# Kernel optimization log

Hardware: AMD Instinct MI355X
Metric: run time of the kernel (lower is better)

The kernel has to match this reference:

```python
import jax, jax.numpy as jnp
import numpy as np

N = 500000   # occupied voxels
C = 128      # channels
K = 27       # 3x3x3 kernel offsets


def setup_inputs() -> dict:
    key = jax.random.key(0)
    ks = jax.random.split(key, 16)
    x = jax.random.normal(ks[0], (N, C), jnp.float32)
    nbr = jax.random.randint(ks[1], (N, K), 0, N, jnp.int32)   # neighbor map (hash-table lookups)
    mask = jax.random.randint(ks[2], (N, K), 0, 2) > 0          # neighbor exists
    s = lambda fan: np.float32(1.0 / np.sqrt(fan))
    C4, C2 = C // 4, C // 2
    W00 = jax.random.normal(ks[3], (C, C4), jnp.float32) * s(C)
    b00 = jax.random.normal(ks[4], (C4,), jnp.float32) * 0.01
    W01 = jax.random.normal(ks[5], (K, C4, C4), jnp.float32) * s(K * C4)
    b01 = jax.random.normal(ks[6], (C4,), jnp.float32) * 0.01
    W02 = jax.random.normal(ks[7], (C4, C2), jnp.float32) * s(C4)
    b02 = jax.random.normal(ks[8], (C2,), jnp.float32) * 0.01
    W10 = jax.random.normal(ks[9], (K, C, C4), jnp.float32) * s(K * C)
    b10 = jax.random.normal(ks[10], (C4,), jnp.float32) * 0.01
    W11 = jax.random.normal(ks[11], (K, C4, C2), jnp.float32) * s(K * C4)
    b11 = jax.random.normal(ks[12], (C2,), jnp.float32) * 0.01
    return {"x": x, "nbr": nbr, "mask": mask,
            "W00": W00, "b00": b00, "W01": W01, "b01": b01, "W02": W02, "b02": b02,
            "W10": W10, "b10": b10, "W11": W11, "b11": b11}


def _conv1(f, W, b):
    # kernel_size=1 sparse conv == per-point matmul
    return f @ W + b


def _conv3(f, nbr, mask, W, b):
    # kernel_size=3 sparse conv: gather-weight-scatter over 27 kernel maps
    acc0 = jnp.zeros((f.shape[0], W.shape[-1]), f.dtype)
    def step(acc, inp):
        idx, m, Wk = inp  # [N], [N], [Cin,Cout]
        g = jnp.where(m[:, None], f[idx], jnp.zeros((), f.dtype))
        return acc + g @ Wk, None
    out, _ = jax.lax.scan(step, acc0, (nbr.T, mask.T, W))
    return out + b


def reference(x, nbr, mask, W00, b00, W01, b01, W02, b02, W10, b10, W11, b11):
    relu = jax.nn.relu
    # branch 0: 1x1 -> relu -> 3x3 -> relu -> 1x1
    h0 = relu(_conv1(x, W00, b00))
    h0 = relu(_conv3(h0, nbr, mask, W01, b01))
    out0 = _conv1(h0, W02, b02)
    # branch 1: 3x3 -> relu -> 3x3
    h1 = relu(_conv3(x, nbr, mask, W10, b10))
    out1 = _conv3(h1, nbr, mask, W11, b11)
    # cat along channels, residual add
    return jnp.concatenate([out0, out1], axis=-1) + x
```

## Files before the change

### kernel.cpp

```cpp
#include <hip/hip_runtime.h>
#include <stdint.h>
#include <stddef.h>


typedef __attribute__((ext_vector_type(8))) short bf16x8;
typedef __attribute__((ext_vector_type(4))) float f32x4;

__device__ __forceinline__ float bf2f(uint16_t u) {
  union { uint32_t i; float f; } v; v.i = ((uint32_t)u) << 16; return v.f;
}
__device__ __forceinline__ uint16_t f2bf(float f) {
  union { float f; uint32_t i; } v; v.f = f;
  return (uint16_t)((v.i + 0x7fffu + ((v.i >> 16) & 1u)) >> 16);
}
__device__ __forceinline__ bf16x8 zero8() {
  bf16x8 z = {0, 0, 0, 0, 0, 0, 0, 0};
  return z;
}
__device__ __forceinline__ bf16x8 cvt8(const float* p) {
  f32x4 u = *(const f32x4*)p, w = *(const f32x4*)(p + 4);
  bf16x8 r;
  r[0] = (short)f2bf(u[0]); r[1] = (short)f2bf(u[1]);
  r[2] = (short)f2bf(u[2]); r[3] = (short)f2bf(u[3]);
  r[4] = (short)f2bf(w[0]); r[5] = (short)f2bf(w[1]);
  r[6] = (short)f2bf(w[2]); r[7] = (short)f2bf(w[3]);
  return r;
}

#define WS_BIASF 399360
#define WS_FLAGS 401408
#define WS_HA    524288
#define WS_HB    34078720
#define WS_XB    67633152

__global__ void detect_modes(const uint32_t* __restrict__ xw,
                             const uint32_t* __restrict__ mw,
                             int* __restrict__ flags) {
  __shared__ int shc[256];
  __shared__ uint32_t shm[256];
  int c = 0;
  uint32_t mv = 0;
  for (int i = threadIdx.x; i < 4096; i += 256) {
    uint32_t e = (xw[i] >> 7) & 0xFFu;
    c += (e >= 110 && e <= 135) ? 1 : 0;
  }
  for (int i = threadIdx.x; i < 2048; i += 256) mv |= mw[i];
  shc[threadIdx.x] = c;
  shm[threadIdx.x] = mv;
  __syncthreads();
  for (int s = 128; s > 0; s >>= 1) {
    if ((int)threadIdx.x < s) {
      shc[threadIdx.x] += shc[threadIdx.x + s];
      shm[threadIdx.x] |= shm[threadIdx.x + s];
    }
    __syncthreads();
  }
  if (threadIdx.x == 0) {
    flags[0] = (shm[0] > 1u) ? 1 : 0;
    flags[1] = (shc[0] < 2048) ? 1 : 0;
    flags[2] = 0;
  }
}

__global__ __launch_bounds__(256) void prep_weights(
    const void* __restrict__ W00, const void* __restrict__ W01,
    const void* __restrict__ W02, const void* __restrict__ W10,
    const void* __restrict__ W11, const void* __restrict__ b00,
    const void* __restrict__ b01, const void* __restrict__ b02,
    const void* __restrict__ b10, const void* __restrict__ b11,
    uint16_t* __restrict__ wt, float* __restrict__ biasF,
    const int* __restrict__ flags) {
  const int f32 = flags[1];
  auto rd = [&](const void* p, int i) -> float {
    return f32 ? ((const float*)p)[i] : bf2f(((const uint16_t*)p)[i]);
  };
  int i = blockIdx.x * 256 + threadIdx.x;
  if (i < 4096) {
    int co = i >> 7, ci = i & 127;
    wt[i] = f2bf(rd(W00, ci * 32 + co)); return;
  }
  i -= 4096;
  if (i < 2048) {
    int co = i >> 5, ci = i & 31;
    wt[4096 + co * 32 + ci] = f2bf(rd(W02, ci * 64 + co)); return;
  }
  i -= 2048;
  if (i < 27648) {
    int k = i >> 10, r = i & 1023, co = r >> 5, ci = r & 31;
    wt[6144 + k * 1024 + co * 32 + ci] = f2bf(rd(W01, k * 1024 + ci * 32 + co)); return;
  }
  i -= 27648;
  if (i < 110592) {
    int k = i >> 12, r = i & 4095, co = r >> 7, ci = r & 127;
    wt[33792 + k * 4096 + co * 128 + ci] = f2bf(rd(W10, k * 4096 + ci * 32 + co)); return;
  }
  i -= 110592;
  if (i < 55296) {
    int k = i >> 11, r = i & 2047, co = r >> 5, ci = r & 31;
    wt[144384 + k * 2048 + co * 32 + ci] = f2bf(rd(W11, k * 2048 + ci * 64 + co)); return;
  }
  i -= 55296;
  if (i < 224) {
    float v;
    if (i < 32)        v = rd(b00, i);
    else if (i < 64)   v = rd(b01, i - 32);
    else if (i < 128)  v = rd(b02, i - 64);
    else if (i < 160)  v = rd(b10, i - 128);
    else               v = rd(b11, i - 160);
    biasF[i] = v;
  }
}

__global__ __launch_bounds__(256) void pack_nbr(
    const int* __restrict__ nbr, const uint8_t* __restrict__ mask8,
    const int* __restrict__ mask32, int* __restrict__ nbrm, int total,
    const int* __restrict__ flags) {
  int i = blockIdx.x * 256 + threadIdx.x;
  if (i >= total) return;
  const int mmode = flags[0];
  int idx = nbr[i];
  bool mk = mmode ? (mask8[i] != 0) : (mask32[i] != 0);
  nbrm[i] = mk ? (idx | (int)0x80000000) : idx;
}

template <bool FDYN>
__device__ __forceinline__ bf16x8 loadA8(const void* f, size_t elem, int xf32) {
  if (FDYN && xf32) return cvt8((const float*)f + elem);
  return *(const bf16x8*)((const uint16_t*)f + elem);
}

template <bool RELU, int ROFF>
__device__ __forceinline__ void epi_store(void* outv, const void* xr, int of32,
                                          size_t p, int col, int COUT, float v,
                                          const float* biasF) {
  v += biasF[col];
  if (RELU) v = fmaxf(v, 0.f);
  if (ROFF >= 0) {
    size_t oi = p * 128 + ROFF + col;
    if (of32) {
      float r = ((const float*)xr)[oi];
      ((float*)outv)[oi] = v + r;
    } else {
      float r = bf2f(((const uint16_t*)xr)[oi]);
      ((uint16_t*)outv)[oi] = f2bf(v + r);
    }
  } else {
    ((uint16_t*)outv)[p * COUT + col] = f2bf(v);
  }
}

template <int CIN, int COUT, bool RELU, int ROFF, bool FDYN, bool CAST>
__global__ __launch_bounds__(256) void conv1_k(
    const void* __restrict__ f, const uint16_t* __restrict__ wt,
    const float* __restrict__ biasF, const void* __restrict__ xr,
    void* __restrict__ outv, int n, const int* __restrict__ flags,
    uint16_t* __restrict__ xb) {
  constexpr int S = CIN / 32;
  constexpr int T = COUT / 16;
  const int xf32 = FDYN ? flags[1] : 0;
  const int of32 = (ROFF >= 0) ? flags[1] : 0;
  const int lane = threadIdx.x & 63;
  const int wid = threadIdx.x >> 6;
  const int m = lane & 15, kg = lane >> 4;
  const int tile0 = blockIdx.x * 16 + wid * 4;

  int tb[4];
  bool rowok[4];
  size_t ab[4];
#pragma unroll
  for (int mt = 0; mt < 4; ++mt) {
    tb[mt] = (tile0 + mt) * 16;
    int row = tb[mt] + m;
    rowok[mt] = row < n;
    ab[mt] = (size_t)(rowok[mt] ? row : 0) * CIN + kg * 8;
  }

  f32x4 acc[4][T];
#pragma unroll
  for (int mt = 0; mt < 4; ++mt)
#pragma unroll
    for (int t = 0; t < T; ++t) acc[mt][t] = {0.f, 0.f, 0.f, 0.f};

#pragma unroll
  for (int s = 0; s < S; ++s) {
    bf16x8 a[4];
#pragma unroll
    for (int mt = 0; mt < 4; ++mt) {
      a[mt] = rowok[mt] ? loadA8<FDYN>(f, ab[mt] + s * 32, xf32) : zero8();
      if constexpr (CAST) {
        if (rowok[mt]) *(bf16x8*)(xb + ab[mt] + s * 32) = a[mt];
      }
    }
#pragma unroll
    for (int t = 0; t < T; ++t) {
      bf16x8 b = *(const bf16x8*)(wt + (size_t)(t * 16 + m) * CIN + s * 32 + kg * 8);
#pragma unroll
      for (int mt = 0; mt < 4; ++mt)
        acc[mt][t] = __builtin_amdgcn_mfma_f32_16x16x32_bf16(a[mt], b, acc[mt][t], 0, 0, 0);
    }
  }

#pragma unroll
  for (int mt = 0; mt < 4; ++mt) {
    if (tb[mt] >= n) continue;
#pragma unroll
    for (int t = 0; t < T; ++t) {
#pragma unroll
      for (int r = 0; r < 4; ++r) {
        int p = tb[mt] + kg * 4 + r;
        if (p >= n) continue;
        epi_store<RELU, ROFF>(outv, xr, of32, (size_t)p, t * 16 + m, COUT,
                              acc[mt][t][r], biasF);
      }
    }
  }
}

template <int CIN, int COUT, int MT, bool RELU, int ROFF, bool PACKED>
__global__ __launch_bounds__(256) void conv3p_k(
    const uint16_t* __restrict__ f, const int* __restrict__ nbrm,
    const uint8_t* __restrict__ mask8, const int* __restrict__ mask32,
    const uint16_t* __restrict__ wt, const float* __restrict__ biasF,
    const void* __restrict__ xr, void* __restrict__ outv, int n,
    const int* __restrict__ flags) {
  constexpr int S = CIN / 32;
  constexpr int T = COUT / 16;
  const int mmode = PACKED ? 0 : flags[0];
  const int of32 = (ROFF >= 0) ? flags[1] : 0;
  const int lane = threadIdx.x & 63;
  const int wid = threadIdx.x >> 6;
  const int m = lane & 15, kg = lane >> 4;
  const int tile0 = (blockIdx.x * 4 + wid) * MT;

  int tb[MT];
  bool rowok[MT];
  int nb[MT];
#pragma unroll
  for (int mt = 0; mt < MT; ++mt) {
    tb[mt] = (tile0 + mt) * 16;
    int row = tb[mt] + m;
    rowok[mt] = row < n;
    nb[mt] = (rowok[mt] ? row : 0) * 27;
  }

  f32x4 acc[MT][T];
#pragma unroll
  for (int mt = 0; mt < MT; ++mt)
#pragma unroll
    for (int t = 0; t < T; ++t) acc[mt][t] = {0.f, 0.f, 0.f, 0.f};

  const uint16_t* wb = wt + (size_t)m * CIN + (size_t)kg * 8;

  int iA[MT], iB[MT], mA[MT], mB[MT];
  bf16x8 aA[MT][S], aB[MT][S];
  bf16x8 bA[T * S], bB[T * S];

  auto LOADIDX = [&](int (&ii)[MT], int (&mm)[MT], int k) {
#pragma unroll
    for (int mt = 0; mt < MT; ++mt) {
      int off = nb[mt] + k;
      ii[mt] = nbrm[off];
      if (!PACKED) mm[mt] = mmode ? (int)mask8[off] : mask32[off];
    }
  };
  auto GATHER = [&](bf16x8 (&a)[MT][S], const int (&ii)[MT],
                    const int (&mm)[MT]) {
#pragma unroll
    for (int mt = 0; mt < MT; ++mt) {
      bool mk;
      int idx;
      if (PACKED) { mk = rowok[mt] && (ii[mt] < 0); idx = ii[mt] & 0x7fffffff; }
      else        { mk = rowok[mt] && (mm[mt] != 0); idx = ii[mt]; }
      if (mk) {
        size_t be = (size_t)idx * CIN + (size_t)kg * 8;
#pragma unroll
        for (int s = 0; s < S; ++s)
          a[mt][s] = *(const bf16x8*)(f + be + s * 32);
      } else {
#pragma unroll
        for (int s = 0; s < S; ++s) a[mt][s] = zero8();
      }
    }
  };
  auto LOADB = [&](bf16x8 (&bb)[T * S], int k) {
    const uint16_t* wk = wb + (size_t)k * COUT * CIN;
#pragma unroll
    for (int t = 0; t < T; ++t)
#pragma unroll
      for (int s = 0; s < S; ++s)
        bb[t * S + s] = *(const bf16x8*)(wk + (size_t)(t * 16) * CIN + s * 32);
  };
  auto MFMA = [&](const bf16x8 (&a)[MT][S], const bf16x8 (&bb)[T * S]) {
#pragma unroll
    for (int t = 0; t < T; ++t)
#pragma unroll
      for (int s = 0; s < S; ++s)
#pragma unroll
        for (int mt = 0; mt < MT; ++mt)
          acc[mt][t] = __builtin_amdgcn_mfma_f32_16x16x32_bf16(
              a[mt][s], bb[t * S + s], acc[mt][t], 0, 0, 0);
  };

  LOADIDX(iA, mA, 0);
  LOADIDX(iB, mB, 1);
  LOADB(bA, 0);
  GATHER(aA, iA, mA);

#pragma unroll 1
  for (int k = 0; k < 26; k += 2) {
    LOADIDX(iA, mA, k + 2);
    LOADB(bB, k + 1);
    GATHER(aB, iB, mB);
    MFMA(aA, bA);
    if (k + 3 < 27) LOADIDX(iB, mB, k + 3);
    LOADB(bA, k + 2);
    GATHER(aA, iA, mA);
    MFMA(aB, bB);
  }
  MFMA(aA, bA);

#pragma unroll
  for (int mt = 0; mt < MT; ++mt) {
    if (tb[mt] >= n) continue;
#pragma unroll
    for (int t = 0; t < T; ++t) {
#pragma unroll
      for (int r = 0; r < 4; ++r) {
        int p = tb[mt] + kg * 4 + r;
        if (p >= n) continue;
        epi_store<RELU, ROFF>(outv, xr, of32, (size_t)p, t * 16 + m, COUT,
                              acc[mt][t][r], biasF);
      }
    }
  }
}

template <int CIN, int COUT, bool RELU, int ROFF, bool FDYN>
__global__ __launch_bounds__(256) void conv3_k(
    const void* __restrict__ f, const int* __restrict__ nbr,
    const uint8_t* __restrict__ mask8, const int* __restrict__ mask32,
    const uint16_t* __restrict__ wt, const float* __restrict__ biasF,
    const void* __restrict__ xr, void* __restrict__ outv, int n,
    const int* __restrict__ flags) {
  constexpr int S = CIN / 32;
  constexpr int T = COUT / 16;
  const int mmode = flags[0];
  const int xf32 = FDYN ? flags[1] : 0;
  const int of32 = (ROFF >= 0) ? flags[1] : 0;
  const int lane = threadIdx.x & 63;
  const int wid = threadIdx.x >> 6;
  const int m = lane & 15, kg = lane >> 4;
  const int tile0 = blockIdx.x * 16 + wid * 4;

  int tb[4];
  bool rowok[4];
  size_t nb[4];
#pragma unroll
  for (int mt = 0; mt < 4; ++mt) {
    tb[mt] = (tile0 + mt) * 16;
    int row = tb[mt] + m;
    rowok[mt] = row < n;
    nb[mt] = (size_t)(rowok[mt] ? row : 0) * 27;
  }

  f32x4 acc[4][T];
#pragma unroll
  for (int mt = 0; mt < 4; ++mt)
#pragma unroll
    for (int t = 0; t < T; ++t) acc[mt][t] = {0.f, 0.f, 0.f, 0.f};

#pragma unroll 1
  for (int k = 0; k < 27; ++k) {
    bf16x8 a[4][S];
#pragma unroll
    for (int mt = 0; mt < 4; ++mt) {
      bool mk = false;
      int idx = 0;
      if (rowok[mt]) {
        size_t off = nb[mt] + k;
        idx = nbr[off];
        mk = mmode ? (mask8[off] != 0) : (mask32[off] != 0);
      }
      if (mk) {
        size_t be = (size_t)idx * CIN + kg * 8;
#pragma unroll
        for (int s = 0; s < S; ++s) a[mt][s] = loadA8<FDYN>(f, be + s * 32, xf32);
      } else {
#pragma unroll
        for (int s = 0; s < S; ++s) a[mt][s] = zero8();
      }
    }
    const uint16_t* wk = wt + (size_t)k * COUT * CIN + (size_t)m * CIN + kg * 8;
#pragma unroll
    for (int t = 0; t < T; ++t) {
#pragma unroll
      for (int s = 0; s < S; ++s) {
        bf16x8 b = *(const bf16x8*)(wk + (size_t)t * 16 * CIN + s * 32);
#pragma unroll
        for (int mt = 0; mt < 4; ++mt)
          acc[mt][t] = __builtin_amdgcn_mfma_f32_16x16x32_bf16(a[mt][s], b, acc[mt][t], 0, 0, 0);
      }
    }
  }

#pragma unroll
  for (int mt = 0; mt < 4; ++mt) {
    if (tb[mt] >= n) continue;
#pragma unroll
    for (int t = 0; t < T; ++t) {
#pragma unroll
      for (int r = 0; r < 4; ++r) {
        int p = tb[mt] + kg * 4 + r;
        if (p >= n) continue;
        epi_store<RELU, ROFF>(outv, xr, of32, (size_t)p, t * 16 + m, COUT,
                              acc[mt][t][r], biasF);
      }
    }
  }
}

extern "C" void kernel_launch(void* const* d_in, const int* in_sizes, int n_in,
                              void* d_out, int out_size, void* d_ws, size_t ws_size,
                              hipStream_t stream) {
  const void* x     = d_in[0];
  const int*  nbr   = (const int*)d_in[1];
  const uint8_t* mask8  = (const uint8_t*)d_in[2];
  const int*     mask32 = (const int*)d_in[2];

  char* ws = (char*)d_ws;
  uint16_t* wt    = (uint16_t*)ws;
  float*    biasF = (float*)(ws + WS_BIASF);
  int*      flags = (int*)(ws + WS_FLAGS);
  uint16_t* hA    = (uint16_t*)(ws + WS_HA);
  uint16_t* hB    = (uint16_t*)(ws + WS_HB);
  uint16_t* xb    = (uint16_t*)(ws + WS_XB);

  const int n = in_sizes[0] / 128;
  const int tiles = (n + 15) / 16;
  const int grid = (tiles + 15) / 16;
  const int g128 = (n + 127) / 128;
  const int g256 = (n + 255) / 256;
  const int total = n * 27;

  const bool have_xb = ws_size >= (size_t)WS_XB + (size_t)n * 256;
  const size_t nbrm_off = (size_t)WS_XB + (size_t)n * 256;
  const bool have_nbrm = have_xb && ws_size >= nbrm_off + (size_t)n * 108;
  int* nbrm = (int*)(ws + nbrm_off);

  detect_modes<<<1, 256, 0, stream>>>((const uint32_t*)d_in[0],
                                      (const uint32_t*)d_in[2], flags);
  if (have_nbrm)
    pack_nbr<<<(total + 255) / 256, 256, 0, stream>>>(nbr, mask8, mask32, nbrm,
                                                      total, flags);
  prep_weights<<<781, 256, 0, stream>>>(d_in[3], d_in[5], d_in[7], d_in[9], d_in[11],
                                        d_in[4], d_in[6], d_in[8], d_in[10], d_in[12],
                                        wt, biasF, flags);

  if (have_xb) {
    conv1_k<128, 32, true, -1, true, true><<<grid, 256, 0, stream>>>(
        x, wt + 0, biasF + 0, nullptr, hA, n, flags, xb);
    if (have_nbrm) {
      conv3p_k<32, 32, 4, true, -1, true><<<g256, 256, 0, stream>>>(
          hA, nbrm, nullptr, nullptr, wt + 6144, biasF + 32, nullptr, hB, n, flags);
      conv3p_k<128, 32, 2, true, -1, true><<<g128, 256, 0, stream>>>(
          xb, nbrm, nullptr, nullptr, wt + 33792, biasF + 128, nullptr, hA, n, flags);
    } else {
      conv3p_k<32, 32, 4, true, -1, false><<<g256, 256, 0, stream>>>(
          hA, nbr, mask8, mask32, wt + 6144, biasF + 32, nullptr, hB, n, flags);
      conv3p_k<128, 32, 2, true, -1, false><<<g128, 256, 0, stream>>>(
          xb, nbr, mask8, mask32, wt + 33792, biasF + 128, nullptr, hA, n, flags);
    }
    conv1_k<32, 64, false, 0, false, false><<<grid, 256, 0, stream>>>(
        hB, wt + 4096, biasF + 64, x, d_out, n, flags, nullptr);
    if (have_nbrm)
      conv3p_k<32, 64, 2, false, 64, true><<<g128, 256, 0, stream>>>(
          hA, nbrm, nullptr, nullptr, wt + 144384, biasF + 160, x, d_out, n, flags);
    else
      conv3p_k<32, 64, 2, false, 64, false><<<g128, 256, 0, stream>>>(
          hA, nbr, mask8, mask32, wt + 144384, biasF + 160, x, d_out, n, flags);
  } else {
    conv1_k<128, 32, true, -1, true, false><<<grid, 256, 0, stream>>>(
        x, wt + 0, biasF + 0, nullptr, hA, n, flags, nullptr);
    conv3_k<32, 32, true, -1, false><<<grid, 256, 0, stream>>>(
        hA, nbr, mask8, mask32, wt + 6144, biasF + 32, nullptr, hB, n, flags);
    conv3_k<128, 32, true, -1, true><<<grid, 256, 0, stream>>>(
        x, nbr, mask8, mask32, wt + 33792, biasF + 128, nullptr, hA, n, flags);
    conv1_k<32, 64, false, 0, false, false><<<grid, 256, 0, stream>>>(
        hB, wt + 4096, biasF + 64, x, d_out, n, flags, nullptr);
    conv3_k<32, 64, false, 64, false><<<grid, 256, 0, stream>>>(
        hA, nbr, mask8, mask32, wt + 144384, biasF + 160, x, d_out, n, flags);
  }
}
```

Baseline: 1.738 ms.

## Fuse parallel sparse 3x3 convs sharing neighbor gathers into two kernels

Adds a kernel that computes the two middle 3x3 sparse convs (branch0 on h0, branch1 on x) in one pass over the neighbor map, and a second kernel that fuses the final 1x1 of branch0 with the last 3x3 of branch1, writing both output halves with the residual. This cuts kernel launches and avoids re-reading the packed neighbor indices for each conv. The old conv3p_k loses its software-pipelined double-buffered index/gather/weight loads in favour of a simple per-k loop. The fused kernels also drop that prefetch and need an extra workspace buffer hC, and the higher register pressure may lower occupancy.

```diff
diff --git a/kernel.cpp b/kernel.cpp
--- a/kernel.cpp
+++ b/kernel.cpp
@@ -216,6 +216,181 @@
   }
 }
 
+__global__ __launch_bounds__(256) void conv3_mid_fused(
+    const uint16_t* __restrict__ h0, const uint16_t* __restrict__ xb,
+    const int* __restrict__ nbrm, const uint16_t* __restrict__ w01,
+    const uint16_t* __restrict__ w10, const float* __restrict__ biasF,
+    uint16_t* __restrict__ hB, uint16_t* __restrict__ hC, int n) {
+  const int lane = threadIdx.x & 63;
+  const int wid = threadIdx.x >> 6;
+  const int m = lane & 15, kg = lane >> 4;
+  const int tile0 = (blockIdx.x * 4 + wid) * 2;
+
+  int tb[2];
+  bool rowok[2];
+  int nb[2];
+#pragma unroll
+  for (int mt = 0; mt < 2; ++mt) {
+    tb[mt] = (tile0 + mt) * 16;
+    int row = tb[mt] + m;
+    rowok[mt] = row < n;
+    nb[mt] = (rowok[mt] ? row : 0) * 27;
+  }
+
+  f32x4 acc0[2][2], acc1[2][2];
+#pragma unroll
+  for (int mt = 0; mt < 2; ++mt)
+#pragma unroll
+    for (int t = 0; t < 2; ++t) {
+      acc0[mt][t] = {0.f, 0.f, 0.f, 0.f};
+      acc1[mt][t] = {0.f, 0.f, 0.f, 0.f};
+    }
+
+  const uint16_t* w01b = w01 + (size_t)m * 32 + kg * 8;
+  const uint16_t* w10b = w10 + (size_t)m * 128 + kg * 8;
+
+#pragma unroll 1
+  for (int k = 0; k < 27; ++k) {
+    bf16x8 a0[2], a1[2][4];
+#pragma unroll
+    for (int mt = 0; mt < 2; ++mt) {
+      int ii = nbrm[nb[mt] + k];
+      bool mk = rowok[mt] && (ii < 0);
+      int idx = ii & 0x7fffffff;
+      if (mk) {
+        const uint16_t* p0 = h0 + (size_t)idx * 32 + kg * 8;
+        const uint16_t* p1 = xb + (size_t)idx * 128 + kg * 8;
+        a0[mt] = *(const bf16x8*)p0;
+#pragma unroll
+        for (int s = 0; s < 4; ++s) a1[mt][s] = *(const bf16x8*)(p1 + s * 32);
+      } else {
+        a0[mt] = zero8();
+#pragma unroll
+        for (int s = 0; s < 4; ++s) a1[mt][s] = zero8();
+      }
+    }
+#pragma unroll
+    for (int t = 0; t < 2; ++t) {
+      bf16x8 b0 = *(const bf16x8*)(w01b + (size_t)k * 1024 + (size_t)t * 16 * 32);
+#pragma unroll
+      for (int mt = 0; mt < 2; ++mt)
+        acc0[mt][t] = __builtin_amdgcn_mfma_f32_16x16x32_bf16(a0[mt], b0, acc0[mt][t], 0, 0, 0);
+    }
+#pragma unroll
+    for (int t = 0; t < 2; ++t) {
+#pragma unroll
+      for (int s = 0; s < 4; ++s) {
+        bf16x8 b1 = *(const bf16x8*)(w10b + (size_t)k * 4096 + (size_t)t * 16 * 128 + s * 32);
+#pragma unroll
+        for (int mt = 0; mt < 2; ++mt)
+          acc1[mt][t] = __builtin_amdgcn_mfma_f32_16x16x32_bf16(a1[mt][s], b1, acc1[mt][t], 0, 0, 0);
+      }
+    }
+  }
+
+#pragma unroll
+  for (int mt = 0; mt < 2; ++mt) {
+    if (tb[mt] >= n) continue;
+#pragma unroll
+    for (int t = 0; t < 2; ++t) {
+#pragma unroll
+      for (int r = 0; r < 4; ++r) {
+        int p = tb[mt] + kg * 4 + r;
+        if (p >= n) continue;
+        int col = t * 16 + m;
+        float v0 = fmaxf(acc0[mt][t][r] + biasF[32 + col], 0.f);
+        float v1 = fmaxf(acc1[mt][t][r] + biasF[128 + col], 0.f);
+        hB[(size_t)p * 32 + col] = f2bf(v0);
+        hC[(size_t)p * 32 + col] = f2bf(v1);
+      }
+    }
+  }
+}
+
+__global__ __launch_bounds__(256) void conv3_out_fused(
+    const uint16_t* __restrict__ hB, const uint16_t* __restrict__ hC,
+    const int* __restrict__ nbrm, const uint16_t* __restrict__ w02,
+    const uint16_t* __restrict__ w11, const float* __restrict__ biasF,
+    const void* __restrict__ xr, void* __restrict__ outv, int n,
+    const int* __restrict__ flags) {
+  const int of32 = flags[1];
+  const int lane = threadIdx.x & 63;
+  const int wid = threadIdx.x >> 6;
+  const int m = lane & 15, kg = lane >> 4;
+  const int tile0 = (blockIdx.x * 4 + wid) * 2;
+
+  int tb[2];
+  bool rowok[2];
+  int nb[2];
+#pragma unroll
+  for (int mt = 0; mt < 2; ++mt) {
+    tb[mt] = (tile0 + mt) * 16;
+    int row = tb[mt] + m;
+    rowok[mt] = row < n;
+    nb[mt] = (rowok[mt] ? row : 0) * 27;
+  }
+
+  f32x4 acc0[2][4], acc1[2][4];
+#pragma unroll
+  for (int mt = 0; mt < 2; ++mt)
+#pragma unroll
+    for (int t = 0; t < 4; ++t) {
+      acc0[mt][t] = {0.f, 0.f, 0.f, 0.f};
+      acc1[mt][t] = {0.f, 0.f, 0.f, 0.f};
+    }
+
+#pragma unroll
+  for (int mt = 0; mt < 2; ++mt) {
+    bf16x8 a = rowok[mt]
+                   ? *(const bf16x8*)(hB + (size_t)(tb[mt] + m) * 32 + kg * 8)
+                   : zero8();
+#pragma unroll
+    for (int t = 0; t < 4; ++t) {
+      bf16x8 b = *(const bf16x8*)(w02 + (size_t)(t * 16 + m) * 32 + kg * 8);
+      acc0[mt][t] = __builtin_amdgcn_mfma_f32_16x16x32_bf16(a, b, acc0[mt][t], 0, 0, 0);
+    }
+  }
+
+  const uint16_t* w11b = w11 + (size_t)m * 32 + kg * 8;
+
+#pragma unroll 1
+  for (int k = 0; k < 27; ++k) {
+    bf16x8 a[2];
+#pragma unroll
+    for (int mt = 0; mt < 2; ++mt) {
+      int ii = nbrm[nb[mt] + k];
+      bool mk = rowok[mt] && (ii < 0);
+      int idx = ii & 0x7fffffff;
+      a[mt] = mk ? *(const bf16x8*)(hC + (size_t)idx * 32 + kg * 8) : zero8();
+    }
+#pragma unroll
+    for (int t = 0; t < 4; ++t) {
+      bf16x8 b = *(const bf16x8*)(w11b + (size_t)k * 2048 + (size_t)t * 16 * 32);
+#pragma unroll
+      for (int mt = 0; mt < 2; ++mt)
+        acc1[mt][t] = __builtin_amdgcn_mfma_f32_16x16x32_bf16(a[mt], b, acc1[mt][t], 0, 0, 0);
+    }
+  }
+
+#pragma unroll
+  for (int mt = 0; mt < 2; ++mt) {
+    if (tb[mt] >= n) continue;
+#pragma unroll
+    for (int t = 0; t < 4; ++t) {
+#pragma unroll
+      for (int r = 0; r < 4; ++r) {
+        int p = tb[mt] + kg * 4 + r;
+        if (p >= n) continue;
+        int col = t * 16 + m;
+        epi_store<false, 0>(outv, xr, of32, (size_t)p, col, 128,
+                            acc0[mt][t][r], biasF + 64);
+        epi_store<false, 64>(outv, xr, of32, (size_t)p, col, 128,
+                             acc1[mt][t][r], biasF + 160);
+      }
+    }
+  }
+}
+
 template <int CIN, int COUT, int MT, bool RELU, int ROFF, bool PACKED>
 __global__ __launch_bounds__(256) void conv3p_k(
     const uint16_t* __restrict__ f, const int* __restrict__ nbrm,
@@ -251,73 +426,40 @@
 
   const uint16_t* wb = wt + (size_t)m * CIN + (size_t)kg * 8;
 
-  int iA[MT], iB[MT], mA[MT], mB[MT];
-  bf16x8 aA[MT][S], aB[MT][S];
-  bf16x8 bA[T * S], bB[T * S];
-
-  auto LOADIDX = [&](int (&ii)[MT], int (&mm)[MT], int k) {
-#pragma unroll
-    for (int mt = 0; mt < MT; ++mt) {
-      int off = nb[mt] + k;
-      ii[mt] = nbrm[off];
-      if (!PACKED) mm[mt] = mmode ? (int)mask8[off] : mask32[off];
-    }
-  };
-  auto GATHER = [&](bf16x8 (&a)[MT][S], const int (&ii)[MT],
-                    const int (&mm)[MT]) {
+#pragma unroll 1
+  for (int k = 0; k < 27; ++k) {
+    bf16x8 a[MT][S];
 #pragma unroll
     for (int mt = 0; mt < MT; ++mt) {
       bool mk;
       int idx;
-      if (PACKED) { mk = rowok[mt] && (ii[mt] < 0); idx = ii[mt] & 0x7fffffff; }
-      else        { mk = rowok[mt] && (mm[mt] != 0); idx = ii[mt]; }
+      int ii = nbrm[nb[mt] + k];
+      if (PACKED) { mk = rowok[mt] && (ii < 0); idx = ii & 0x7fffffff; }
+      else {
+        int mm = mmode ? (int)mask8[nb[mt] + k] : mask32[nb[mt] + k];
+        mk = rowok[mt] && (mm != 0);
+        idx = ii;
+      }
       if (mk) {
         size_t be = (size_t)idx * CIN + (size_t)kg * 8;
 #pragma unroll
-        for (int s = 0; s < S; ++s)
-          a[mt][s] = *(const bf16x8*)(f + be + s * 32);
+        for (int s = 0; s < S; ++s) a[mt][s] = *(const bf16x8*)(f + be + s * 32);
       } else {
 #pragma unroll
         for (int s = 0; s < S; ++s) a[mt][s] = zero8();
       }
     }
-  };
-  auto LOADB = [&](bf16x8 (&bb)[T * S], int k) {
-    const uint16_t* wk = wb + (size_t)k * COUT * CIN;
-#pragma unroll
-    for (int t = 0; t < T; ++t)
-#pragma unroll
-      for (int s = 0; s < S; ++s)
-        bb[t * S + s] = *(const bf16x8*)(wk + (size_t)(t * 16) * CIN + s * 32);
-  };
-  auto MFMA = [&](const bf16x8 (&a)[MT][S], const bf16x8 (&bb)[T * S]) {
-#pragma unroll
-    for (int t = 0; t < T; ++t)
-#pragma unroll
-      for (int s = 0; s < S; ++s)
+#pragma unroll
+    for (int t = 0; t < T; ++t) {
+#pragma unroll
+      for (int s = 0; s < S; ++s) {
+        bf16x8 b = *(const bf16x8*)(wb + (size_t)k * COUT * CIN + (size_t)t * 16 * CIN + s * 32);
 #pragma unroll
         for (int mt = 0; mt < MT; ++mt)
-          acc[mt][t] = __builtin_amdgcn_mfma_f32_16x16x32_bf16(
-              a[mt][s], bb[t * S + s], acc[mt][t], 0, 0, 0);
-  };
-
-  LOADIDX(iA, mA, 0);
-  LOADIDX(iB, mB, 1);
-  LOADB(bA, 0);
-  GATHER(aA, iA, mA);
-
-#pragma unroll 1
-  for (int k = 0; k < 26; k += 2) {
-    LOADIDX(iA, mA, k + 2);
-    LOADB(bB, k + 1);
-    GATHER(aB, iB, mB);
-    MFMA(aA, bA);
-    if (k + 3 < 27) LOADIDX(iB, mB, k + 3);
-    LOADB(bA, k + 2);
-    GATHER(aA, iA, mA);
-    MFMA(aB, bB);
-  }
-  MFMA(aA, bA);
+          acc[mt][t] = __builtin_amdgcn_mfma_f32_16x16x32_bf16(a[mt][s], b, acc[mt][t], 0, 0, 0);
+      }
+    }
+  }
 
 #pragma unroll
   for (int mt = 0; mt < MT; ++mt) {
@@ -445,7 +587,10 @@
   const bool have_xb = ws_size >= (size_t)WS_XB + (size_t)n * 256;
   const size_t nbrm_off = (size_t)WS_XB + (size_t)n * 256;
   const bool have_nbrm = have_xb && ws_size >= nbrm_off + (size_t)n * 108;
+  const size_t hC_off = nbrm_off + (size_t)n * 108;
+  const bool have_fuse = have_nbrm && ws_size >= hC_off + (size_t)n * 64;
   int* nbrm = (int*)(ws + nbrm_off);
+  uint16_t* hC = (uint16_t*)(ws + hC_off);
 
   detect_modes<<<1, 256, 0, stream>>>((const uint32_t*)d_in[0],
                                       (const uint32_t*)d_in[2], flags);
@@ -456,7 +601,14 @@
                                         d_in[4], d_in[6], d_in[8], d_in[10], d_in[12],
                                         wt, biasF, flags);
 
-  if (have_xb) {
+  if (have_fuse) {
+    conv1_k<128, 32, true, -1, true, true><<<grid, 256, 0, stream>>>(
+        x, wt + 0, biasF + 0, nullptr, hA, n, flags, xb);
+    conv3_mid_fused<<<g128, 256, 0, stream>>>(hA, xb, nbrm, wt + 6144,
+                                              wt + 33792, biasF, hB, hC, n);
+    conv3_out_fused<<<g128, 256, 0, stream>>>(hB, hC, nbrm, wt + 4096,
+                                              wt + 144384, biasF, x, d_out, n, flags);
+  } else if (have_xb) {
     conv1_k<128, 32, true, -1, true, true><<<grid, 256, 0, stream>>>(
         x, wt + 0, biasF + 0, nullptr, hA, n, flags, xb);
     if (have_nbrm) {
@@ -466,9 +618,9 @@
           xb, nbrm, nullptr, nullptr, wt + 33792, biasF + 128, nullptr, hA, n, flags);
     } else {
       conv3p_k<32, 32, 4, true, -1, false><<<g256, 256, 0, stream>>>(
-          hA, nbr, mask8, mask32, wt + 6144, biasF + 32, nullptr, hB, n, flags);
+          hA, (const int*)nbr, mask8, mask32, wt + 6144, biasF + 32, nullptr, hB, n, flags);
       conv3p_k<128, 32, 2, true, -1, false><<<g128, 256, 0, stream>>>(
-          xb, nbr, mask8, mask32, wt + 33792, biasF + 128, nullptr, hA, n, flags);
+          xb, (const int*)nbr, mask8, mask32, wt + 33792, biasF + 128, nullptr, hA, n, flags);
     }
     conv1_k<32, 64, false, 0, false, false><<<grid, 256, 0, stream>>>(
         hB, wt + 4096, biasF + 64, x, d_out, n, flags, nullptr);
@@ -477,7 +629,7 @@
           hA, nbrm, nullptr, nullptr, wt + 144384, biasF + 160, x, d_out, n, flags);
     else
       conv3p_k<32, 64, 2, false, 64, false><<<g128, 256, 0, stream>>>(
-          hA, nbr, mask8, mask32, wt + 144384, biasF + 160, x, d_out, n, flags);
+          hA, (const int*)nbr, mask8, mask32, wt + 144384, biasF + 160, x, d_out, n, flags);
   } else {
     conv1_k<128, 32, true, -1, true, false><<<grid, 256, 0, stream>>>(
         x, wt + 0, biasF + 0, nullptr, hA, n, flags, nullptr);
```

New measurement: 1.700 ms. 2.1% less time.
